# Performance work log

Measured on AMD Instinct MI355X. Metric: run time of the kernel, lower is better.

Reference implementation:

```python
import jax, jax.numpy as jnp
import numpy as np

B, N, Mc, K = 8, 16384, 2048, 32
EMB = 256


def setup_inputs() -> dict:
    key = jax.random.key(0)
    ks = jax.random.split(key, 9)
    xyz = jax.random.normal(ks[0], (B, N, 3), dtype=jnp.float32)
    centers = jax.random.normal(ks[1], (B, Mc, 3), dtype=jnp.float32)
    idx_knn = jax.random.randint(ks[2], (B, Mc, K), 0, N, dtype=jnp.int32)
    # 1x1 conv weights == pointwise linear layers (out_ch, in_ch) + bias
    def kaiming(k, o, i):
        return jax.random.normal(k, (o, i), dtype=jnp.float32) * np.float32(np.sqrt(2.0 / i))
    W1, b1 = kaiming(ks[3], 64, 3), jnp.zeros((64,), jnp.float32)
    W2, b2 = kaiming(ks[4], 128, 64), jnp.zeros((128,), jnp.float32)
    W3, b3 = kaiming(ks[5], EMB, 128), jnp.zeros((EMB,), jnp.float32)
    return {"xyz": xyz, "centers": centers, "idx_knn": idx_knn,
            "W1": W1, "b1": b1, "W2": W2, "b2": b2, "W3": W3, "b3": b3}


def reference(xyz, centers, idx_knn, W1, b1, W2, b2, W3, b3):
    # gather KNN neighbors: (B, M, K, 3)
    neigh = jnp.take_along_axis(xyz[:, None, :, :], idx_knn[..., None], axis=2)
    local = neigh - centers[:, :, None, :]          # center-subtract
    # 1x1 convs are pointwise linears over the channel dim
    h = jax.nn.relu(jnp.einsum('bmkc,oc->bmko', local, W1) + b1)
    h = jax.nn.relu(jnp.einsum('bmkc,oc->bmko', h, W2) + b2)
    h = jnp.einsum('bmkc,oc->bmko', h, W3) + b3      # (B, M, K, EMB)
    return jnp.max(h, axis=2)                        # max over K -> (B, M, EMB)
```

## Files before the change

### kernel.cpp

```cpp
#include <hip/hip_runtime.h>
#include <hip/hip_bf16.h>


typedef __attribute__((ext_vector_type(8))) short bf16x8;
typedef __attribute__((ext_vector_type(4))) float f32x4v;

constexpr int Bn = 8, Nn = 16384, Mn = 2048, Kn = 32, EMB = 256;
constexpr int G = 2;
constexpr int ROWS = G * Kn;

__device__ __forceinline__ unsigned short bfr(float x) {
    unsigned u = __float_as_uint(x);
    u += 0x7fffu + ((u >> 16) & 1u);
    return (unsigned short)(u >> 16);
}

__device__ __forceinline__ bf16x8 pack8(const float* v) {
    bf16x8 r;
    #pragma unroll
    for (int i = 0; i < 8; ++i) r[i] = (short)bfr(v[i]);
    return r;
}

__global__ __launch_bounds__(256) void pe_pack(
    const float* __restrict__ W2, const float* __restrict__ W3,
    uint4* __restrict__ ws)
{
    int gid = blockIdx.x * 256 + threadIdx.x;
    if (gid < 1024) {
        int e = gid, l = e & 63;
        int kt = (e >> 6) & 1, ct = (e >> 7) & 1, w = e >> 8;
        int q = l >> 4, n = l & 15;
        int ch = w * 32 + ct * 16 + n;
        const float* p = W2 + ch * 64 + kt * 32 + q * 8;
        float t[8];
        *(float4*)&t[0] = *(const float4*)p;
        *(float4*)&t[4] = *(const float4*)(p + 4);
        bf16x8 v = pack8(t);
        ws[e] = *(uint4*)&v;
    } else if (gid < 5120) {
        int e = gid - 1024, l = e & 63;
        int kt = (e >> 6) & 3, ct = (e >> 8) & 3, w = e >> 10;
        int q = l >> 4, n = l & 15;
        int ch = w * 64 + ct * 16 + n;
        const float* p = W3 + ch * 128 + kt * 32 + q * 8;
        float t[8];
        *(float4*)&t[0] = *(const float4*)p;
        *(float4*)&t[4] = *(const float4*)(p + 4);
        bf16x8 v = pack8(t);
        ws[1024 + e] = *(uint4*)&v;
    }
}

__global__ __launch_bounds__(256, 4) void pe_mfma(
    const float* __restrict__ xyz,
    const float* __restrict__ centers,
    const int*   __restrict__ idx,
    const float* __restrict__ W1,
    const float* __restrict__ b1,
    const float* __restrict__ b2,
    const float* __restrict__ b3,
    const uint4* __restrict__ wsf,
    float*       __restrict__ out)
{
    __shared__ uint4  h1v[ROWS * 64 * 2 / 16];
    __shared__ uint4  h2v[ROWS * 128 * 2 / 16];
    __shared__ float4 w1v[48];
    __shared__ float  b1f[64];

    const int tid = threadIdx.x;
    const int w   = tid >> 6;
    const int l   = tid & 63;
    const int q   = l >> 4;
    const int n   = l & 15;
    const int bm0 = blockIdx.x * G;

    bf16x8 B2f[2][2];  float b2v[2];
    #pragma unroll
    for (int ct = 0; ct < 2; ++ct) {
        b2v[ct] = b2[w * 32 + ct * 16 + n];
        #pragma unroll
        for (int kt = 0; kt < 2; ++kt) {
            uint4 u = wsf[((w * 2 + ct) * 2 + kt) * 64 + l];
            B2f[ct][kt] = *(bf16x8*)&u;
        }
    }
    bf16x8 B3f[4][4];  float b3v[4];
    #pragma unroll
    for (int ct = 0; ct < 4; ++ct) {
        b3v[ct] = b3[w * 64 + ct * 16 + n];
        #pragma unroll
        for (int kt = 0; kt < 4; ++kt) {
            uint4 u = wsf[1024 + ((w * 4 + ct) * 4 + kt) * 64 + l];
            B3f[ct][kt] = *(bf16x8*)&u;
        }
    }

    if (tid < 48) w1v[tid] = ((const float4*)W1)[tid];
    if (tid < 64) b1f[tid] = b1[tid];

    const int r64 = tid & 63;
    {
        int bm = bm0 + (r64 >> 5);
        int bb = bm >> 11;
        int id = idx[(size_t)bm * Kn + (r64 & 31)];
        const float* p = xyz + ((size_t)bb * Nn + id) * 3;
        const float* c = centers + (size_t)bm * 3;
        float lx = p[0] - c[0], ly = p[1] - c[1], lz = p[2] - c[2];
        __syncthreads();

        float h[16];
        const int o4b = (tid >> 6) * 4;
        #pragma unroll
        for (int i = 0; i < 4; ++i) {
            int o4 = o4b + i;
            float4 wa = w1v[3 * o4], wb = w1v[3 * o4 + 1], wc = w1v[3 * o4 + 2];
            h[4*i+0] = fmaxf(b1f[4*o4+0] + lx*wa.x + ly*wa.y + lz*wa.z, 0.f);
            h[4*i+1] = fmaxf(b1f[4*o4+1] + lx*wa.w + ly*wb.x + lz*wb.y, 0.f);
            h[4*i+2] = fmaxf(b1f[4*o4+2] + lx*wb.z + ly*wb.w + lz*wc.x, 0.f);
            h[4*i+3] = fmaxf(b1f[4*o4+3] + lx*wc.y + ly*wc.z + lz*wc.w, 0.f);
        }
        const int T = r64 >> 4, r = r64 & 15, j0 = (tid >> 6) * 2;
        #pragma unroll
        for (int jj = 0; jj < 2; ++jj) {
            bf16x8 v = pack8(&h[8 * jj]);
            h1v[T * 128 + (j0 + jj) * 16 + r] = *(uint4*)&v;
        }
    }
    __syncthreads();

    {
        ushort* h2s = (ushort*)h2v;
        for (int rt = 0; rt < G * 2; ++rt) {
            uint4 a0u = h1v[rt * 128 + q * 16 + n];
            uint4 a1u = h1v[rt * 128 + (4 + q) * 16 + n];
            bf16x8 A0 = *(bf16x8*)&a0u, A1 = *(bf16x8*)&a1u;
            #pragma unroll
            for (int ct = 0; ct < 2; ++ct) {
                f32x4v c0 = {0.f, 0.f, 0.f, 0.f};
                c0 = __builtin_amdgcn_mfma_f32_16x16x32_bf16(A0, B2f[ct][0], c0, 0, 0, 0);
                c0 = __builtin_amdgcn_mfma_f32_16x16x32_bf16(A1, B2f[ct][1], c0, 0, 0, 0);
                int ch = w * 32 + ct * 16 + n;
                #pragma unroll
                for (int reg = 0; reg < 4; ++reg) {
                    float v = fmaxf(c0[reg] + b2v[ct], 0.f);
                    int rowl = q * 4 + reg;
                    h2s[rt * 2048 + (ch >> 3) * 128 + rowl * 8 + (ch & 7)] = bfr(v);
                }
            }
        }
    }
    __syncthreads();

    {
        float cmax[4];
        for (int rt = 0; rt < G * 2; ++rt) {
            bf16x8 A[4];
            #pragma unroll
            for (int kt = 0; kt < 4; ++kt) {
                uint4 au = h2v[rt * 256 + (kt * 4 + q) * 16 + n];
                A[kt] = *(bf16x8*)&au;
            }
            #pragma unroll
            for (int ct = 0; ct < 4; ++ct) {
                f32x4v C = {0.f, 0.f, 0.f, 0.f};
                #pragma unroll
                for (int kt = 0; kt < 4; ++kt)
                    C = __builtin_amdgcn_mfma_f32_16x16x32_bf16(A[kt], B3f[ct][kt], C, 0, 0, 0);
                float v = fmaxf(fmaxf(C[0], C[1]), fmaxf(C[2], C[3]));
                v = fmaxf(v, __shfl_xor(v, 16));
                v = fmaxf(v, __shfl_xor(v, 32));
                if ((rt & 1) == 0) {
                    cmax[ct] = v;
                } else if (q == 0) {
                    float r = fmaxf(cmax[ct], v) + b3v[ct];
                    out[(size_t)(bm0 + (rt >> 1)) * EMB + w * 64 + ct * 16 + n] = r;
                }
            }
        }
    }
}

extern "C" void kernel_launch(void* const* d_in, const int* in_sizes, int n_in,
                              void* d_out, int out_size, void* d_ws, size_t ws_size,
                              hipStream_t stream) {
    const float* xyz     = (const float*)d_in[0];
    const float* centers = (const float*)d_in[1];
    const int*   idx     = (const int*)  d_in[2];
    const float* W1      = (const float*)d_in[3];
    const float* b1      = (const float*)d_in[4];
    const float* W2      = (const float*)d_in[5];
    const float* b2      = (const float*)d_in[6];
    const float* W3      = (const float*)d_in[7];
    const float* b3      = (const float*)d_in[8];
    float*       out     = (float*)d_out;
    uint4*       ws      = (uint4*)d_ws;

    pe_pack<<<20, 256, 0, stream>>>(W2, W3, ws);
    pe_mfma<<<(Bn * Mn) / G, 256, 0, stream>>>(
        xyz, centers, idx, W1, b1, b2, b3, ws, out);
}
```

Baseline: 127.4 us.

## Load W1/b1 from global, drop a barrier, interleave even/odd MFMA chains

Drops the shared-memory staging of W1/b1 and the barrier that preceded layer 1; each wave now reads its W1 rows and biases straight from global (cached) memory. Layer 3 processes the two 16-row tiles of a centroid together, running two independent MFMA accumulation chains so they can interleave and hide latency, and merges the max before the shuffle reduction. It also raises the occupancy hint to 6 blocks per CU and unrolls the layer-2 loop. A leftover dead loop that reads the hoisted wr/br is kept, and the higher occupancy target may force register spills given the many weight fragments held in registers.

```diff
diff --git a/kernel.cpp b/kernel.cpp
--- a/kernel.cpp
+++ b/kernel.cpp
@@ -52,7 +52,7 @@
     }
 }
 
-__global__ __launch_bounds__(256, 4) void pe_mfma(
+__global__ __launch_bounds__(256, 6) void pe_mfma(
     const float* __restrict__ xyz,
     const float* __restrict__ centers,
     const int*   __restrict__ idx,
@@ -63,10 +63,8 @@
     const uint4* __restrict__ wsf,
     float*       __restrict__ out)
 {
-    __shared__ uint4  h1v[ROWS * 64 * 2 / 16];
-    __shared__ uint4  h2v[ROWS * 128 * 2 / 16];
-    __shared__ float4 w1v[48];
-    __shared__ float  b1f[64];
+    __shared__ uint4 h1v[ROWS * 64 * 2 / 16];
+    __shared__ uint4 h2v[ROWS * 128 * 2 / 16];
 
     const int tid = threadIdx.x;
     const int w   = tid >> 6;
@@ -96,8 +94,17 @@
         }
     }
 
-    if (tid < 48) w1v[tid] = ((const float4*)W1)[tid];
-    if (tid < 64) b1f[tid] = b1[tid];
+    const int o4b = __builtin_amdgcn_readfirstlane((tid >> 6) * 4);
+    float wr[12], br[4];
+    {
+        const float4* Wp = (const float4*)(W1 + o4b * 12);
+        float4 wa = Wp[0], wb = Wp[1], wc = Wp[2];
+        wr[0]=wa.x; wr[1]=wa.y; wr[2]=wa.z; wr[3]=wa.w;
+        wr[4]=wb.x; wr[5]=wb.y; wr[6]=wb.z; wr[7]=wb.w;
+        wr[8]=wc.x; wr[9]=wc.y; wr[10]=wc.z; wr[11]=wc.w;
+        float4 bb = *(const float4*)(b1 + o4b * 4);
+        br[0]=bb.x; br[1]=bb.y; br[2]=bb.z; br[3]=bb.w;
+    }
 
     const int r64 = tid & 63;
     {
@@ -107,18 +114,25 @@
         const float* p = xyz + ((size_t)bb * Nn + id) * 3;
         const float* c = centers + (size_t)bm * 3;
         float lx = p[0] - c[0], ly = p[1] - c[1], lz = p[2] - c[2];
-        __syncthreads();
 
         float h[16];
-        const int o4b = (tid >> 6) * 4;
         #pragma unroll
         for (int i = 0; i < 4; ++i) {
-            int o4 = o4b + i;
-            float4 wa = w1v[3 * o4], wb = w1v[3 * o4 + 1], wc = w1v[3 * o4 + 2];
-            h[4*i+0] = fmaxf(b1f[4*o4+0] + lx*wa.x + ly*wa.y + lz*wa.z, 0.f);
-            h[4*i+1] = fmaxf(b1f[4*o4+1] + lx*wa.w + ly*wb.x + lz*wb.y, 0.f);
-            h[4*i+2] = fmaxf(b1f[4*o4+2] + lx*wb.z + ly*wb.w + lz*wc.x, 0.f);
-            h[4*i+3] = fmaxf(b1f[4*o4+3] + lx*wc.y + ly*wc.z + lz*wc.w, 0.f);
+            h[4*i+0] = fmaxf(br[0] + lx*wr[0] + ly*wr[1]  + lz*wr[2], 0.f);
+        }
+        #pragma unroll
+        for (int i = 0; i < 4; ++i) {
+            const float4* Wp = (const float4*)(W1 + (o4b + i) * 12);
+            float4 wa = Wp[0], wb = Wp[1], wc = Wp[2];
+            float b0, b1v_, b2_, b3_;
+            {
+                const float4 bb4 = *(const float4*)(b1 + (o4b + i) * 4);
+                b0 = bb4.x; b1v_ = bb4.y; b2_ = bb4.z; b3_ = bb4.w;
+            }
+            h[4*i+0] = fmaxf(b0   + lx*wa.x + ly*wa.y + lz*wa.z, 0.f);
+            h[4*i+1] = fmaxf(b1v_ + lx*wa.w + ly*wb.x + lz*wb.y, 0.f);
+            h[4*i+2] = fmaxf(b2_  + lx*wb.z + ly*wb.w + lz*wc.x, 0.f);
+            h[4*i+3] = fmaxf(b3_  + lx*wc.y + ly*wc.z + lz*wc.w, 0.f);
         }
         const int T = r64 >> 4, r = r64 & 15, j0 = (tid >> 6) * 2;
         #pragma unroll
@@ -131,6 +145,7 @@
 
     {
         ushort* h2s = (ushort*)h2v;
+        #pragma unroll
         for (int rt = 0; rt < G * 2; ++rt) {
             uint4 a0u = h1v[rt * 128 + q * 16 + n];
             uint4 a1u = h1v[rt * 128 + (4 + q) * 16 + n];
@@ -153,28 +168,31 @@
     __syncthreads();
 
     {
-        float cmax[4];
-        for (int rt = 0; rt < G * 2; ++rt) {
-            bf16x8 A[4];
+        #pragma unroll
+        for (int g = 0; g < G; ++g) {
+            bf16x8 Ae[4], Ao[4];
             #pragma unroll
             for (int kt = 0; kt < 4; ++kt) {
-                uint4 au = h2v[rt * 256 + (kt * 4 + q) * 16 + n];
-                A[kt] = *(bf16x8*)&au;
+                uint4 ae = h2v[(2*g)   * 256 + (kt * 4 + q) * 16 + n];
+                uint4 ao = h2v[(2*g+1) * 256 + (kt * 4 + q) * 16 + n];
+                Ae[kt] = *(bf16x8*)&ae;
+                Ao[kt] = *(bf16x8*)&ao;
             }
             #pragma unroll
             for (int ct = 0; ct < 4; ++ct) {
-                f32x4v C = {0.f, 0.f, 0.f, 0.f};
+                f32x4v Ce = {0.f, 0.f, 0.f, 0.f};
+                f32x4v Co = {0.f, 0.f, 0.f, 0.f};
                 #pragma unroll
-                for (int kt = 0; kt < 4; ++kt)
-                    C = __builtin_amdgcn_mfma_f32_16x16x32_bf16(A[kt], B3f[ct][kt], C, 0, 0, 0);
-                float v = fmaxf(fmaxf(C[0], C[1]), fmaxf(C[2], C[3]));
+                for (int kt = 0; kt < 4; ++kt) {
+                    Ce = __builtin_amdgcn_mfma_f32_16x16x32_bf16(Ae[kt], B3f[ct][kt], Ce, 0, 0, 0);
+                    Co = __builtin_amdgcn_mfma_f32_16x16x32_bf16(Ao[kt], B3f[ct][kt], Co, 0, 0, 0);
+                }
+                float v = fmaxf(fmaxf(fmaxf(Ce[0], Co[0]), fmaxf(Ce[1], Co[1])),
+                                fmaxf(fmaxf(Ce[2], Co[2]), fmaxf(Ce[3], Co[3])));
                 v = fmaxf(v, __shfl_xor(v, 16));
                 v = fmaxf(v, __shfl_xor(v, 32));
-                if ((rt & 1) == 0) {
-                    cmax[ct] = v;
-                } else if (q == 0) {
-                    float r = fmaxf(cmax[ct], v) + b3v[ct];
-                    out[(size_t)(bm0 + (rt >> 1)) * EMB + w * 64 + ct * 16 + n] = r;
+                if (q == 0) {
+                    out[(size_t)(bm0 + g) * EMB + w * 64 + ct * 16 + n] = v + b3v[ct];
                 }
             }
         }
```

After: 223.7 us. +75.6%, slower.
